# Kernel optimization log

Hardware: AMD Instinct MI355X
Metric: run time of the kernel (lower is better)

Reference implementation:

```python
import jax, jax.numpy as jnp
import numpy as np

N_LAYERS = 3
N_HEADS = 8
N_HIDDEN = 16  # hidden_dim // n_heads
HIDDEN = 128
SLOPE = 0.2


def setup_inputs() -> dict:
    key = jax.random.key(0)
    ks = jax.random.split(key, 7)
    B, N, Din, Dh = 4, 512, 2, HIDDEN
    node_features = jax.random.normal(ks[0], (B, N, Din), dtype=jnp.float32)
    adj = jax.random.randint(ks[1], (B, N, N), 0, 2).astype(jnp.int32)
    adj = jnp.maximum(adj, jnp.eye(N, dtype=jnp.int32)[None])  # self loops -> no empty softmax rows
    s = 1.0 / np.sqrt(Dh)
    W_in = jax.random.normal(ks[2], (Din, Dh), dtype=jnp.float32) * (1.0 / np.sqrt(Din))
    W_l = jax.random.normal(ks[3], (N_LAYERS, Dh, N_HEADS * N_HIDDEN), dtype=jnp.float32) * s
    W_r = jax.random.normal(ks[4], (N_LAYERS, Dh, N_HEADS * N_HIDDEN), dtype=jnp.float32) * s
    attn_a = jax.random.normal(ks[5], (N_LAYERS, N_HIDDEN), dtype=jnp.float32) * (1.0 / np.sqrt(N_HIDDEN))
    W_out = jax.random.normal(ks[6], (Dh, 1), dtype=jnp.float32) * s
    return {"node_features": node_features, "adj": adj, "W_in": W_in,
            "W_l": W_l, "W_r": W_r, "attn_a": attn_a, "W_out": W_out}


def _gatv2_layer(h, adj, Wl, Wr, a):
    # h: [B,N,Dh]; adj: [B,N,N] int; Wl/Wr: [Dh, H*F]; a: [F]
    B, N, _ = h.shape
    g_l = (h @ Wl).reshape(B, N, N_HEADS, N_HIDDEN)
    g_r = (h @ Wr).reshape(B, N, N_HEADS, N_HIDDEN)
    # torch: g_sum[b,i,j] = g_l[b,j] + g_r[b,i]  (repeat vs repeat_interleave)
    g_sum = g_r[:, :, None, :, :] + g_l[:, None, :, :, :]  # [B,N,N,H,F]
    e = jnp.einsum('bijhf,f->bijh', jax.nn.leaky_relu(g_sum, SLOPE), a)  # [B,N,N,H]
    e = jnp.where(adj[..., None] == 0, -jnp.inf, e)
    att = jax.nn.softmax(e, axis=2)  # softmax over neighbors j
    out = jnp.einsum('bijh,bjhf->bihf', att, g_r)  # aggregate g_r (per source)
    return out.reshape(B, N, N_HEADS * N_HIDDEN)


def reference(node_features, adj, W_in, W_l, W_r, attn_a, W_out):
    h = node_features @ W_in  # [B,N,128]
    for i in range(N_LAYERS):
        h = _gatv2_layer(h, adj, W_l[i], W_r[i], attn_a[i])
    return h @ W_out  # [B,N,1]
```

## Files before the change

kernel.cpp:

```cpp
#include <hip/hip_runtime.h>
#include <hip/hip_bf16.h>
#include <cstdint>
#include <math.h>

#define NB 4
#define NN 512
#define DH 128
#define NHEADS 8
#define NHID 16
#define SLOPE 0.2f
#define ITILE 32
#define SENTINEL -1e30f

__global__ __launch_bounds__(256) void pack_adj_kernel(
    const int* __restrict__ adj, uint32_t* __restrict__ adjb)
{
    const int t   = threadIdx.x;
    const int row = blockIdx.x * 16 + (t >> 4);
    const int w   = t & 15;
    const int4* p = (const int4*)(adj + (size_t)row * NN + w * 32);
    uint32_t m = 0;
#pragma unroll
    for (int c = 0; c < 8; ++c) {
        const int4 v = p[c];
        m |= (v.x != 0 ? 1u : 0u) << (c * 4 + 0);
        m |= (v.y != 0 ? 1u : 0u) << (c * 4 + 1);
        m |= (v.z != 0 ? 1u : 0u) << (c * 4 + 2);
        m |= (v.w != 0 ? 1u : 0u) << (c * 4 + 3);
    }
    adjb[(size_t)row * 16 + w] = m;
}

__global__ __launch_bounds__(256) void proj_kernel(
    const float* __restrict__ h, const float* __restrict__ X,
    const float* __restrict__ Win,
    const float* __restrict__ Wl, const float* __restrict__ Wr,
    float* __restrict__ gl, float* __restrict__ gr)
{
    __shared__ __align__(16) float s_h[8][DH];
    const int bn0 = blockIdx.x * 8;
    const int b   = bn0 >> 9;
    const int n0  = bn0 & 511;
    const int t   = threadIdx.x;

    if (X) {
        if (t < DH) {
            const float w0 = Win[t], w1 = Win[DH + t];
#pragma unroll
            for (int r = 0; r < 8; ++r) {
                const float x0 = X[(bn0 + r) * 2 + 0];
                const float x1 = X[(bn0 + r) * 2 + 1];
                s_h[r][t] = x0 * w0 + x1 * w1;
            }
        }
    } else {
        for (int idx = t; idx < 8 * DH; idx += 256)
            s_h[idx >> 7][idx & 127] = h[(size_t)bn0 * DH + idx];
    }
    __syncthreads();

    const float* W = (t < DH) ? Wl : Wr;
    float*       g = (t < DH) ? gl : gr;
    const int f128 = t & 127;
    float acc[8] = {};
    for (int k = 0; k < DH; k += 4) {
        const float w0 = W[(k + 0) * DH + f128];
        const float w1 = W[(k + 1) * DH + f128];
        const float w2 = W[(k + 2) * DH + f128];
        const float w3 = W[(k + 3) * DH + f128];
#pragma unroll
        for (int r = 0; r < 8; ++r) {
            const float4 hv = *(const float4*)&s_h[r][k];
            acc[r] += hv.x * w0 + hv.y * w1 + hv.z * w2 + hv.w * w3;
        }
    }
    const int hh = f128 >> 4, f = f128 & 15;
    float* dst = g + ((size_t)(b * NHEADS + hh) * NN + n0) * NHID + f;
#pragma unroll
    for (int r = 0; r < 8; ++r)
        dst[r * NHID] = acc[r];
}

__global__ __launch_bounds__(512) void attn_kernel(
    const float* __restrict__ gl, const float* __restrict__ gr,
    const uint32_t* __restrict__ adjb, const float* __restrict__ a_vec,
    float* __restrict__ h_out,
    const float* __restrict__ Wout, float* __restrict__ out)
{
    __shared__ __align__(16) float smem[17504];
    float* s_gl  = smem;
    float* s_gr  = smem + 8192;
    float* s_acc = smem;
    float* s_m   = smem + 16384;
    float* s_l   = smem + 16912;
    float* s_M   = smem + 17440;
    float* s_inv = smem + 17472;

    const int blk = blockIdx.x;
    const int it  = blk & 15;
    const int bh  = blk >> 4;
    const int b   = bh >> 3;
    const int hh  = bh & 7;
    const int i0  = it * ITILE;
    const int t   = threadIdx.x;
    const int il  = t & 31;
    const int js  = t >> 5;

    {
        const float4* pgl = (const float4*)(gl + (size_t)bh * NN * NHID);
        const float4* pgr = (const float4*)(gr + (size_t)bh * NN * NHID);
        float4* dl = (float4*)s_gl;
        float4* dr = (float4*)s_gr;
#pragma unroll
        for (int k = 0; k < 4; ++k) {
            dl[k * 512 + t] = pgl[k * 512 + t];
            dr[k * 512 + t] = pgr[k * 512 + t];
        }
    }
    float a[16];
    {
        const float4* pa = (const float4*)a_vec;
#pragma unroll
        for (int q = 0; q < 4; ++q) {
            const float4 v = pa[q];
            a[4*q] = v.x; a[4*q+1] = v.y; a[4*q+2] = v.z; a[4*q+3] = v.w;
        }
    }
    const uint32_t mask = adjb[((size_t)(b * NN + i0 + il)) * 16 + js];
    __syncthreads();

    float gri[16];
    {
        const float4* pr = (const float4*)(s_gr + (i0 + il) * NHID);
#pragma unroll
        for (int q = 0; q < 4; ++q) {
            const float4 v = pr[q];
            gri[4*q] = v.x; gri[4*q+1] = v.y; gri[4*q+2] = v.z; gri[4*q+3] = v.w;
        }
    }

    float m = SENTINEL, l = 0.f;
    float acc[16];
#pragma unroll
    for (int f = 0; f < 16; ++f) acc[f] = 0.f;

    const int jbase = js * 32;
    for (int jc = 0; jc < 32; jc += 4) {
        float sc[4];
#pragma unroll
        for (int k = 0; k < 4; ++k) {
            const int jj = jc + k;
            const float4* pg = (const float4*)(s_gl + (jbase + jj) * NHID);
            float s = 0.f;
#pragma unroll
            for (int q = 0; q < 4; ++q) {
                const float4 g = pg[q];
                float v;
                v = g.x + gri[4*q+0]; v = fmaxf(v, SLOPE * v); s += v * a[4*q+0];
                v = g.y + gri[4*q+1]; v = fmaxf(v, SLOPE * v); s += v * a[4*q+1];
                v = g.z + gri[4*q+2]; v = fmaxf(v, SLOPE * v); s += v * a[4*q+2];
                v = g.w + gri[4*q+3]; v = fmaxf(v, SLOPE * v); s += v * a[4*q+3];
            }
            sc[k] = ((mask >> jj) & 1u) ? s : SENTINEL;
        }
        const float m4   = fmaxf(fmaxf(sc[0], sc[1]), fmaxf(sc[2], sc[3]));
        const float newm = fmaxf(m, m4);
        const float corr = __expf(m - newm);
        l *= corr;
#pragma unroll
        for (int f = 0; f < 16; ++f) acc[f] *= corr;
        float p[4];
#pragma unroll
        for (int k = 0; k < 4; ++k) p[k] = __expf(sc[k] - newm);
        l += p[0] + p[1] + p[2] + p[3];
#pragma unroll
        for (int k = 0; k < 4; ++k) {
            const float4* pg = (const float4*)(s_gr + (jbase + jc + k) * NHID);
#pragma unroll
            for (int q = 0; q < 4; ++q) {
                const float4 g = pg[q];
                acc[4*q+0] += p[k] * g.x; acc[4*q+1] += p[k] * g.y;
                acc[4*q+2] += p[k] * g.z; acc[4*q+3] += p[k] * g.w;
            }
        }
        m = newm;
    }

    s_m[js * 33 + il] = m;
    s_l[js * 33 + il] = l;
    __syncthreads();

    if (t < 32) {
        float M = SENTINEL;
#pragma unroll
        for (int k = 0; k < 16; ++k) M = fmaxf(M, s_m[k * 33 + t]);
        float L = 0.f;
#pragma unroll
        for (int k = 0; k < 16; ++k) L += s_l[k * 33 + t] * __expf(s_m[k * 33 + t] - M);
        s_M[t]   = M;
        s_inv[t] = 1.f / L;
    }
    __syncthreads();

    {
        const float scale = __expf(m - s_M[il]) * s_inv[il];
        float* dst = s_acc + (js * 32 + il) * 17;
#pragma unroll
        for (int f = 0; f < 16; ++f) dst[f] = acc[f] * scale;
    }
    __syncthreads();

    {
        const int i = t >> 4, f = t & 15;
        float o = 0.f;
#pragma unroll
        for (int k = 0; k < 16; ++k) o += s_acc[(k * 32 + i) * 17 + f];
        if (Wout) {
            float v = o * Wout[hh * NHID + f];
#pragma unroll
            for (int off = 8; off; off >>= 1) v += __shfl_xor(v, off);
            if (f == 0) atomicAdd(out + b * NN + i0 + i, v);
        } else {
            h_out[((size_t)(b * NN + i0 + i)) * DH + hh * NHID + f] = o;
        }
    }
}

extern "C" void kernel_launch(void* const* d_in, const int* in_sizes, int n_in,
                              void* d_out, int out_size, void* d_ws, size_t ws_size,
                              hipStream_t stream) {
    const float* X    = (const float*)d_in[0];
    const int*   adj  = (const int*)  d_in[1];
    const float* Win  = (const float*)d_in[2];
    const float* Wl   = (const float*)d_in[3];
    const float* Wr   = (const float*)d_in[4];
    const float* Aa   = (const float*)d_in[5];
    const float* Wout = (const float*)d_in[6];
    float* out = (float*)d_out;

    float*    ws   = (float*)d_ws;
    float*    h    = ws;
    float*    gl   = ws + 262144;
    float*    gr   = ws + 524288;
    uint32_t* adjb = (uint32_t*)(ws + 786432);

    pack_adj_kernel<<<NB * NN / 16, 256, 0, stream>>>(adj, adjb);
    hipMemsetAsync(out, 0, (size_t)out_size * sizeof(float), stream);

    for (int l = 0; l < 3; ++l) {
        proj_kernel<<<NB * NN / 8, 256, 0, stream>>>(
            h, (l == 0) ? X : nullptr, Win,
            Wl + (size_t)l * DH * DH, Wr + (size_t)l * DH * DH, gl, gr);
        const bool last = (l == 2);
        attn_kernel<<<NB * NHEADS * (NN / ITILE), 512, 0, stream>>>(
            gl, gr, adjb, Aa + l * NHID, h,
            last ? Wout : nullptr, out);
    }
}
```

Measured before the change: 181.0 us.

## Double attention row tile per block and switch to two-pass register softmax

Raises ITILE from 32 to 64 so each thread scores two target rows against the same neighbour rows. Each LDS read of gl/gr is reused twice, and the per-block staging of the full gl/gr head slice is spread over twice as many rows. The online-softmax rescaling is replaced by computing all 32 scores into registers, taking the max, then exponentiating and accumulating. The cost is much higher register pressure and half as many blocks, which may reduce occupancy and latency hiding.

```diff
diff --git a/kernel.cpp b/kernel.cpp
--- a/kernel.cpp
+++ b/kernel.cpp
@@ -9,7 +9,7 @@
 #define NHEADS 8
 #define NHID 16
 #define SLOPE 0.2f
-#define ITILE 32
+#define ITILE 64
 #define SENTINEL -1e30f
 
 __global__ __launch_bounds__(256) void pack_adj_kernel(
@@ -87,24 +87,25 @@
     float* __restrict__ h_out,
     const float* __restrict__ Wout, float* __restrict__ out)
 {
-    __shared__ __align__(16) float smem[17504];
+    __shared__ __align__(16) float smem[19648];
     float* s_gl  = smem;
     float* s_gr  = smem + 8192;
     float* s_acc = smem;
-    float* s_m   = smem + 16384;
-    float* s_l   = smem + 16912;
-    float* s_M   = smem + 17440;
-    float* s_inv = smem + 17472;
+    float* s_m   = smem + 17408;
+    float* s_l   = smem + 18464;
+    float* s_M   = smem + 19520;
+    float* s_inv = smem + 19584;
 
     const int blk = blockIdx.x;
-    const int it  = blk & 15;
-    const int bh  = blk >> 4;
+    const int it  = blk & 7;
+    const int bh  = blk >> 3;
     const int b   = bh >> 3;
     const int hh  = bh & 7;
     const int i0  = it * ITILE;
     const int t   = threadIdx.x;
     const int il  = t & 31;
     const int js  = t >> 5;
+    const int jbase = js * 32;
 
     {
         const float4* pgl = (const float4*)(gl + (size_t)bh * NN * NHID);
@@ -117,111 +118,109 @@
             dr[k * 512 + t] = pgr[k * 512 + t];
         }
     }
-    float a[16];
-    {
-        const float4* pa = (const float4*)a_vec;
+    const float4* a_g = (const float4*)a_vec;
+    const float4 a4[4] = { a_g[0], a_g[1], a_g[2], a_g[3] };
+    const uint32_t mask0 = adjb[((size_t)(b * NN + i0 + il))      * 16 + js];
+    const uint32_t mask1 = adjb[((size_t)(b * NN + i0 + il + 32)) * 16 + js];
+    __syncthreads();
+
+    float gri0[16], gri1[16];
+    {
+        const float4* p0 = (const float4*)(s_gr + (i0 + il) * NHID);
+        const float4* p1 = (const float4*)(s_gr + (i0 + il + 32) * NHID);
 #pragma unroll
         for (int q = 0; q < 4; ++q) {
-            const float4 v = pa[q];
-            a[4*q] = v.x; a[4*q+1] = v.y; a[4*q+2] = v.z; a[4*q+3] = v.w;
-        }
-    }
-    const uint32_t mask = adjb[((size_t)(b * NN + i0 + il)) * 16 + js];
-    __syncthreads();
-
-    float gri[16];
-    {
-        const float4* pr = (const float4*)(s_gr + (i0 + il) * NHID);
+            const float4 v0 = p0[q], v1 = p1[q];
+            gri0[4*q] = v0.x; gri0[4*q+1] = v0.y; gri0[4*q+2] = v0.z; gri0[4*q+3] = v0.w;
+            gri1[4*q] = v1.x; gri1[4*q+1] = v1.y; gri1[4*q+2] = v1.z; gri1[4*q+3] = v1.w;
+        }
+    }
+
+    float sc0[32], sc1[32];
+#pragma unroll
+    for (int jj = 0; jj < 32; ++jj) {
+        const float4* pg = (const float4*)(s_gl + (jbase + jj) * NHID);
+        float s0 = 0.f, s1 = 0.f;
 #pragma unroll
         for (int q = 0; q < 4; ++q) {
-            const float4 v = pr[q];
-            gri[4*q] = v.x; gri[4*q+1] = v.y; gri[4*q+2] = v.z; gri[4*q+3] = v.w;
-        }
-    }
-
-    float m = SENTINEL, l = 0.f;
-    float acc[16];
-#pragma unroll
-    for (int f = 0; f < 16; ++f) acc[f] = 0.f;
-
-    const int jbase = js * 32;
-    for (int jc = 0; jc < 32; jc += 4) {
-        float sc[4];
-#pragma unroll
-        for (int k = 0; k < 4; ++k) {
-            const int jj = jc + k;
-            const float4* pg = (const float4*)(s_gl + (jbase + jj) * NHID);
-            float s = 0.f;
-#pragma unroll
-            for (int q = 0; q < 4; ++q) {
-                const float4 g = pg[q];
-                float v;
-                v = g.x + gri[4*q+0]; v = fmaxf(v, SLOPE * v); s += v * a[4*q+0];
-                v = g.y + gri[4*q+1]; v = fmaxf(v, SLOPE * v); s += v * a[4*q+1];
-                v = g.z + gri[4*q+2]; v = fmaxf(v, SLOPE * v); s += v * a[4*q+2];
-                v = g.w + gri[4*q+3]; v = fmaxf(v, SLOPE * v); s += v * a[4*q+3];
-            }
-            sc[k] = ((mask >> jj) & 1u) ? s : SENTINEL;
-        }
-        const float m4   = fmaxf(fmaxf(sc[0], sc[1]), fmaxf(sc[2], sc[3]));
-        const float newm = fmaxf(m, m4);
-        const float corr = __expf(m - newm);
-        l *= corr;
-#pragma unroll
-        for (int f = 0; f < 16; ++f) acc[f] *= corr;
-        float p[4];
-#pragma unroll
-        for (int k = 0; k < 4; ++k) p[k] = __expf(sc[k] - newm);
-        l += p[0] + p[1] + p[2] + p[3];
-#pragma unroll
-        for (int k = 0; k < 4; ++k) {
-            const float4* pg = (const float4*)(s_gr + (jbase + jc + k) * NHID);
-#pragma unroll
-            for (int q = 0; q < 4; ++q) {
-                const float4 g = pg[q];
-                acc[4*q+0] += p[k] * g.x; acc[4*q+1] += p[k] * g.y;
-                acc[4*q+2] += p[k] * g.z; acc[4*q+3] += p[k] * g.w;
-            }
-        }
-        m = newm;
-    }
-
-    s_m[js * 33 + il] = m;
-    s_l[js * 33 + il] = l;
-    __syncthreads();
-
-    if (t < 32) {
+            const float4 g = pg[q];
+            const float4 av = a4[q];
+            float v;
+            v = g.x + gri0[4*q+0]; v = fmaxf(v, SLOPE * v); s0 += v * av.x;
+            v = g.y + gri0[4*q+1]; v = fmaxf(v, SLOPE * v); s0 += v * av.y;
+            v = g.z + gri0[4*q+2]; v = fmaxf(v, SLOPE * v); s0 += v * av.z;
+            v = g.w + gri0[4*q+3]; v = fmaxf(v, SLOPE * v); s0 += v * av.w;
+            v = g.x + gri1[4*q+0]; v = fmaxf(v, SLOPE * v); s1 += v * av.x;
+            v = g.y + gri1[4*q+1]; v = fmaxf(v, SLOPE * v); s1 += v * av.y;
+            v = g.z + gri1[4*q+2]; v = fmaxf(v, SLOPE * v); s1 += v * av.z;
+            v = g.w + gri1[4*q+3]; v = fmaxf(v, SLOPE * v); s1 += v * av.w;
+        }
+        sc0[jj] = ((mask0 >> jj) & 1u) ? s0 : SENTINEL;
+        sc1[jj] = ((mask1 >> jj) & 1u) ? s1 : SENTINEL;
+    }
+    float m0 = SENTINEL, m1 = SENTINEL;
+#pragma unroll
+    for (int jj = 0; jj < 32; ++jj) { m0 = fmaxf(m0, sc0[jj]); m1 = fmaxf(m1, sc1[jj]); }
+
+    float acc0[16] = {}, acc1[16] = {};
+    float l0 = 0.f, l1 = 0.f;
+#pragma unroll
+    for (int jj = 0; jj < 32; ++jj) {
+        const float p0 = __expf(sc0[jj] - m0);
+        const float p1 = __expf(sc1[jj] - m1);
+        l0 += p0; l1 += p1;
+        const float4* pg = (const float4*)(s_gr + (jbase + jj) * NHID);
+#pragma unroll
+        for (int q = 0; q < 4; ++q) {
+            const float4 g = pg[q];
+            acc0[4*q+0] += p0 * g.x; acc0[4*q+1] += p0 * g.y;
+            acc0[4*q+2] += p0 * g.z; acc0[4*q+3] += p0 * g.w;
+            acc1[4*q+0] += p1 * g.x; acc1[4*q+1] += p1 * g.y;
+            acc1[4*q+2] += p1 * g.z; acc1[4*q+3] += p1 * g.w;
+        }
+    }
+    s_m[js * 66 + il]      = m0;  s_l[js * 66 + il]      = l0;
+    s_m[js * 66 + il + 32] = m1;  s_l[js * 66 + il + 32] = l1;
+    __syncthreads();
+
+    if (t < 64) {
         float M = SENTINEL;
 #pragma unroll
-        for (int k = 0; k < 16; ++k) M = fmaxf(M, s_m[k * 33 + t]);
+        for (int k = 0; k < 16; ++k) M = fmaxf(M, s_m[k * 66 + t]);
         float L = 0.f;
 #pragma unroll
-        for (int k = 0; k < 16; ++k) L += s_l[k * 33 + t] * __expf(s_m[k * 33 + t] - M);
+        for (int k = 0; k < 16; ++k) L += s_l[k * 66 + t] * __expf(s_m[k * 66 + t] - M);
         s_M[t]   = M;
         s_inv[t] = 1.f / L;
     }
     __syncthreads();
 
     {
-        const float scale = __expf(m - s_M[il]) * s_inv[il];
-        float* dst = s_acc + (js * 32 + il) * 17;
-#pragma unroll
-        for (int f = 0; f < 16; ++f) dst[f] = acc[f] * scale;
-    }
-    __syncthreads();
-
-    {
-        const int i = t >> 4, f = t & 15;
-        float o = 0.f;
-#pragma unroll
-        for (int k = 0; k < 16; ++k) o += s_acc[(k * 32 + i) * 17 + f];
-        if (Wout) {
-            float v = o * Wout[hh * NHID + f];
-#pragma unroll
-            for (int off = 8; off; off >>= 1) v += __shfl_xor(v, off);
-            if (f == 0) atomicAdd(out + b * NN + i0 + i, v);
-        } else {
-            h_out[((size_t)(b * NN + i0 + i)) * DH + hh * NHID + f] = o;
+        const float f0s = __expf(m0 - s_M[il])      * s_inv[il];
+        const float f1s = __expf(m1 - s_M[il + 32]) * s_inv[il + 32];
+        float* d0 = s_acc + (js * 64 + il) * 17;
+        float* d1 = s_acc + (js * 64 + il + 32) * 17;
+#pragma unroll
+        for (int f = 0; f < 16; ++f) { d0[f] = acc0[f] * f0s; d1[f] = acc1[f] * f1s; }
+    }
+    __syncthreads();
+
+    {
+        const int f = t & 15;
+#pragma unroll
+        for (int half = 0; half < 2; ++half) {
+            const int i = (t >> 4) + half * 32;
+            float o = 0.f;
+#pragma unroll
+            for (int k = 0; k < 16; ++k) o += s_acc[(k * 64 + i) * 17 + f];
+            if (Wout) {
+                float v = o * Wout[hh * NHID + f];
+#pragma unroll
+                for (int off = 8; off; off >>= 1) v += __shfl_xor(v, off);
+                if (f == 0) atomicAdd(out + b * NN + i0 + i, v);
+            } else {
+                h_out[((size_t)(b * NN + i0 + i)) * DH + hh * NHID + f] = o;
+            }
         }
     }
 }
```

After: 367.7 us. 103% more time.
